# Optimization experiments

Hardware: AMD Instinct MI355X
Metric: run time of the kernel (lower is better)

## Reference

```python
import jax, jax.numpy as jnp
import numpy as np

B, N, DIM, H = 4, 128, 512, 8
EPS = 1e-5

def _lin(k, fan_in, fan_out):
    kw, kb = jax.random.split(k)
    w = jax.random.normal(kw, (fan_in, fan_out), jnp.float32) * 0.02
    b = jax.random.normal(kb, (fan_out,), jnp.float32) * 0.02
    return w, b

def setup_inputs() -> dict:
    key = jax.random.key(0)
    ks = jax.random.split(key, 12)
    node_features = jax.random.normal(ks[0], (B, N, DIM), jnp.float32)
    edge_features = jax.random.normal(ks[1], (B, N, N, DIM), jnp.float32)
    adjacency_weights = jax.random.uniform(ks[2], (B, N, N), jnp.float32)
    Wn_w, Wn_b = _lin(ks[3], DIM, DIM)
    We1_w, We1_b = _lin(ks[4], 3 * DIM, DIM)
    We2_w, We2_b = _lin(ks[5], DIM, H)
    Wm_w, Wm_b = _lin(ks[6], DIM, DIM)
    Wu1_w, Wu1_b = _lin(ks[7], 3 * DIM, DIM)
    Wu2_w, Wu2_b = _lin(ks[8], DIM, DIM)
    Wo_w, Wo_b = _lin(ks[9], DIM, DIM)
    ln_g = jnp.ones((DIM,), jnp.float32)
    ln_b = jnp.zeros((DIM,), jnp.float32)
    return dict(node_features=node_features, edge_features=edge_features,
                adjacency_weights=adjacency_weights,
                Wn_w=Wn_w, Wn_b=Wn_b, We1_w=We1_w, We1_b=We1_b,
                We2_w=We2_w, We2_b=We2_b, Wm_w=Wm_w, Wm_b=Wm_b,
                Wu1_w=Wu1_w, Wu1_b=Wu1_b, Wu2_w=Wu2_w, Wu2_b=Wu2_b,
                Wo_w=Wo_w, Wo_b=Wo_b, ln_g=ln_g, ln_b=ln_b)

def _layernorm(x, g, b):
    mu = jnp.mean(x, axis=-1, keepdims=True)
    var = jnp.var(x, axis=-1, keepdims=True)
    return (x - mu) * jax.lax.rsqrt(var + EPS) * g + b

def reference(node_features, edge_features, adjacency_weights,
              Wn_w, Wn_b, We1_w, We1_b, We2_w, We2_b, Wm_w, Wm_b,
              Wu1_w, Wu1_b, Wu2_w, Wu2_b, Wo_w, Wo_b, ln_g, ln_b):
    b, n, d = node_features.shape
    h = node_features @ Wn_w + Wn_b                       # (B,N,D)
    h_i = jnp.broadcast_to(h[:, :, None, :], (b, n, n, d))
    h_j = jnp.broadcast_to(h[:, None, :, :], (b, n, n, d))
    edge_input = jnp.concatenate([h_i, h_j, edge_features], axis=-1)  # (B,N,N,3D)
    # edge attention MLP
    e = jax.nn.leaky_relu(edge_input @ We1_w + We1_b, negative_slope=0.2)
    attn = e @ We2_w + We2_b                              # (B,N,N,H)
    attn = jax.nn.softmax(attn, axis=2)                   # softmax over j
    attn = attn * adjacency_weights[..., None]
    # messages: W_msg applied to h_j == W_msg(h) broadcast; aggregate with mean attn
    messages = h @ Wm_w + Wm_b                            # (B,N,D)
    attn_mean = jnp.mean(attn, axis=-1)                   # (B,N,N)
    aggregated = jnp.einsum('bij,bjd->bid', attn_mean, messages)
    updated_nodes = _layernorm(node_features + (aggregated @ Wo_w + Wo_b), ln_g, ln_b)
    # edge update MLP (exact GELU as in torch default)
    u = jax.nn.gelu(edge_input @ Wu1_w + Wu1_b, approximate=False)
    updated_edges = edge_features + (u @ Wu2_w + Wu2_b)
    return updated_nodes, updated_edges
```

## Files before the change

### kernel.cpp

```cpp
#include <hip/hip_runtime.h>
#include <hip/hip_bf16.h>


typedef __bf16  bf16x8 __attribute__((ext_vector_type(8)));
typedef float   f32x4  __attribute__((ext_vector_type(4)));
typedef __hip_bfloat16 bfloat;

#define AS1 __attribute__((address_space(1)))
#define AS3 __attribute__((address_space(3)))

__device__ __forceinline__ void g2l16(const void* g, void* l) {
  __builtin_amdgcn_global_load_lds((AS1 void*)g, (AS3 void*)l, 16, 0, 0);
}

__device__ __forceinline__ float ldf(const void* p, size_t i, int f) {
  return f ? ((const float*)p)[i] : __bfloat162float(((const bfloat*)p)[i]);
}
__device__ __forceinline__ void stf(void* p, size_t i, float v, int f) {
  if (f) ((float*)p)[i] = v;
  else   ((bfloat*)p)[i] = __float2bfloat16(v);
}

__device__ __forceinline__ float gelu_f(float x) {
  float y = 0.7978845608028654f * (x + 0.044715f * x * x * x);
  float e = __expf(2.0f * y);
  float t = 1.0f - 2.0f / (e + 1.0f);
  return 0.5f * x * (1.0f + t);
}

__global__ __launch_bounds__(256) void detect_dtype(const unsigned short* nu, int* flag) {
  __shared__ int bad;
  if (threadIdx.x == 0) bad = 0;
  __syncthreads();
  int local = 0;
  for (int i = threadIdx.x; i < 4096; i += 256) {
    int ex = (nu[i] >> 7) & 0xFF;
    if (ex >= 0xC0) local = 1;
  }
  if (local) atomicOr(&bad, 1);
  __syncthreads();
  if (threadIdx.x == 0) *flag = bad;
}

__global__ __launch_bounds__(256) void cvt_edge(const float* E, const int* flag, void* dout) {
  if (*flag == 0) return;
  const int e = blockIdx.x & 7;
  const int x = blockIdx.x >> 3;
  const int m = x >> 5;
  const int h = (x >> 4) & 1;
  const int s = x & 15;
  const int c = 2 * e + 16 * m + h;
  const int t = threadIdx.x;
  const int rloc = s * 4 + (t >> 6);
  const int c8 = t & 63;
  const float* src = E + ((size_t)c * 64 + rloc) * 512 + (size_t)c8 * 8;
  f32x4 lo = *(const f32x4*)src;
  f32x4 hi = *(const f32x4*)(src + 4);
  bf16x8 v;
  v[0] = (__bf16)lo[0]; v[1] = (__bf16)lo[1]; v[2] = (__bf16)lo[2]; v[3] = (__bf16)lo[3];
  v[4] = (__bf16)hi[0]; v[5] = (__bf16)hi[1]; v[6] = (__bf16)hi[2]; v[7] = (__bf16)hi[3];
  char* eb = (char*)dout + 1048576;
  *(bf16x8*)(eb + (size_t)c * 131072 + (size_t)rloc * 1024 + (size_t)c8 * 16) = v;
}

__global__ __launch_bounds__(256) void transpose3(const void* We1, const void* Wu1,
                                                  const void* Wu2, const int* flag,
                                                  bfloat* WtA, bfloat* WtB, bfloat* WtC) {
  const int f = *flag;
  int idx = blockIdx.x * 256 + threadIdx.x;
  int m = idx >> 18;
  int r = idx & 262143;
  int n = r >> 9, k = r & 511;
  size_t si = (size_t)k * 512 + n;
  float v;
  bfloat* dst;
  if (m == 0)      { v = ldf(We1, 524288 + si, f); dst = WtA; }
  else if (m == 1) { v = ldf(Wu1, 524288 + si, f); dst = WtB; }
  else             { v = ldf(Wu2, si, f);          dst = WtC; }
  dst[(size_t)n * 512 + k] = __float2bfloat16(v);
}

__global__ __launch_bounds__(256) void small_gemm(const void* A, int amode, const void* W,
                                                  size_t woff, const void* bias,
                                                  const int* flag, float* out) {
  const int f = *flag;
  const int af = amode ? 1 : f;
  __shared__ float sA[4][512];
  const int t = threadIdx.x;
  const int r0 = blockIdx.x * 4;
  for (int idx = t; idx < 2048; idx += 256)
    sA[idx >> 9][idx & 511] = ldf(A, (size_t)(r0 + (idx >> 9)) * 512 + (idx & 511), af);
  __syncthreads();
  float acc0[4] = {0.f, 0.f, 0.f, 0.f}, acc1[4] = {0.f, 0.f, 0.f, 0.f};
#pragma unroll 4
  for (int k = 0; k < 512; ++k) {
    float w0 = ldf(W, woff + (size_t)k * 512 + t, f);
    float w1 = ldf(W, woff + (size_t)k * 512 + t + 256, f);
#pragma unroll
    for (int r = 0; r < 4; ++r) {
      acc0[r] += sA[r][k] * w0;
      acc1[r] += sA[r][k] * w1;
    }
  }
  float b0 = bias ? ldf(bias, t, f) : 0.f;
  float b1 = bias ? ldf(bias, t + 256, f) : 0.f;
#pragma unroll
  for (int r = 0; r < 4; ++r) {
    out[(size_t)(r0 + r) * 512 + t] = acc0[r] + b0;
    out[(size_t)(r0 + r) * 512 + t + 256] = acc1[r] + b1;
  }
}

__global__ __launch_bounds__(256) void fused5(const float* h, const void* We1, const void* We1b,
                                              const void* Wu1, const void* Wu1b, const void* Wm,
                                              const void* Wmb, const int* flag, float* P1,
                                              float* Q1, float* P2, float* Q2, float* msgv) {
  const int f = *flag;
  const void* W;
  size_t woff = 0;
  const void* bias = nullptr;
  float* out;
  switch (blockIdx.y) {
    case 0:  W = We1; bias = We1b; out = P1; break;
    case 1:  W = We1; woff = 262144; out = Q1; break;
    case 2:  W = Wu1; bias = Wu1b; out = P2; break;
    case 3:  W = Wu1; woff = 262144; out = Q2; break;
    default: W = Wm;  bias = Wmb;  out = msgv; break;
  }
  __shared__ float sA[4][512];
  const int t = threadIdx.x;
  const int r0 = blockIdx.x * 4;
  for (int idx = t; idx < 2048; idx += 256)
    sA[idx >> 9][idx & 511] = h[(size_t)(r0 + (idx >> 9)) * 512 + (idx & 511)];
  __syncthreads();
  float acc0[4] = {0.f, 0.f, 0.f, 0.f}, acc1[4] = {0.f, 0.f, 0.f, 0.f};
#pragma unroll 4
  for (int k = 0; k < 512; ++k) {
    float w0 = ldf(W, woff + (size_t)k * 512 + t, f);
    float w1 = ldf(W, woff + (size_t)k * 512 + t + 256, f);
#pragma unroll
    for (int r = 0; r < 4; ++r) {
      acc0[r] += sA[r][k] * w0;
      acc1[r] += sA[r][k] * w1;
    }
  }
  float b0 = bias ? ldf(bias, t, f) : 0.f;
  float b1 = bias ? ldf(bias, t + 256, f) : 0.f;
#pragma unroll
  for (int r = 0; r < 4; ++r) {
    out[(size_t)(r0 + r) * 512 + t] = acc0[r] + b0;
    out[(size_t)(r0 + r) * 512 + t + 256] = acc1[r] + b1;
  }
}

__global__ __launch_bounds__(256) void k3_edge_mlp(const void* E, const bfloat* WtA,
                                                   const bfloat* WtB, const float* P1,
                                                   const float* Q1, const float* P2,
                                                   const float* Q2, const void* We2,
                                                   const int* flag, float* logits4, void* dout) {
  const int f = *flag;
  __shared__ __align__(16) char smem[53248];
  f32x4 acc[4][4];
#pragma unroll
  for (int mi = 0; mi < 4; ++mi)
#pragma unroll
    for (int ni = 0; ni < 4; ++ni) acc[mi][ni] = (f32x4){0.f, 0.f, 0.f, 0.f};

  const int idx0 = blockIdx.x;
  const int bm = (idx0 >> 6) * 8 + (idx0 & 7);
  const int bn = (idx0 >> 3) & 7;
  const bool attn = bn < 4;
  const bfloat* Bg = attn ? WtA + (size_t)bn * 65536 : WtB + (size_t)(bn - 4) * 65536;
  const bfloat* Eb = (const bfloat*)E;
  const char* eb = (const char*)dout + 1048576;

  const int t = threadIdx.x;
  const int lane = t & 63;
  const int wave = t >> 6;
  const int wrow = wave >> 1, wcol = wave & 1;
  const int l15 = lane & 15;
  const int q = lane >> 4;
  const int blockcol = (attn ? bn : (bn - 4)) * 128;

  const int row0 = t >> 2, p0 = t & 3, g0 = p0 ^ (row0 & 3);
  const int row1 = 64 + row0, g1 = p0 ^ (row1 & 3);
  const char* srcB0 = (const char*)Bg + ((size_t)row0 * 512 + g0 * 8) * 2;
  const char* srcB1 = (const char*)Bg + ((size_t)row1 * 512 + g1 * 8) * 2;
  const char* srcA0;
  const char* srcA1;
  const int gr0 = bm * 128 + row0, gr1 = gr0 + 64;
  if (f) {
    srcA0 = eb + (size_t)(gr0 >> 6) * 131072 + (size_t)(gr0 & 63) * 1024 + (size_t)g0 * 16;
    srcA1 = eb + (size_t)(gr1 >> 6) * 131072 + (size_t)(gr1 & 63) * 1024 + (size_t)g1 * 16;
  } else {
    srcA0 = (const char*)Eb + ((size_t)gr0 * 512 + g0 * 8) * 2;
    srcA1 = (const char*)Eb + ((size_t)gr1 * 512 + g1 * 8) * 2;
  }
  const int dst0 = wave * 1024;
  const int dst1 = 4096 + wave * 1024;

  auto stage = [&](int kt2, int sel2) {
    char* dA = smem + sel2 * 8192;
    char* dB = smem + 24576 + sel2 * 8192;
    const int koff = kt2 * 64;
    g2l16(srcA0 + koff, dA + dst0);
    g2l16(srcA1 + koff, dA + dst1);
    g2l16(srcB0 + koff, dB + dst0);
    g2l16(srcB1 + koff, dB + dst1);
  };

  stage(0, 0);
  stage(1, 1);

  if (attn) {
    for (int idx = t; idx < 2048; idx += 256) {
      const int n = idx >> 7, k = idx & 127;
      float v = (n < 8) ? ldf(We2, (size_t)(blockcol + k) * 8 + n, f) : 0.f;
      *(bfloat*)(smem + 49152 + (size_t)n * 256 + (((k >> 3) ^ n) * 16) + (k & 7) * 2) =
          __float2bfloat16(v);
    }
  }

  const int fA = (wrow * 64 + l15) * 64 + ((q ^ (l15 & 3)) * 16);
  const int fB = (wcol * 64 + l15) * 64 + ((q ^ (l15 & 3)) * 16);

#pragma unroll
  for (int kt = 0; kt < 16; ++kt) {
    if (kt < 15) asm volatile("s_waitcnt vmcnt(4)" ::: "memory");
    else         asm volatile("s_waitcnt vmcnt(0)" ::: "memory");
    __builtin_amdgcn_s_barrier();
    if (kt < 14) stage(kt + 2, (kt + 2) % 3);
    const char* A = smem + (kt % 3) * 8192;
    const char* B = smem + 24576 + (kt % 3) * 8192;
    bf16x8 afr[4], bfr[4];
#pragma unroll
    for (int mi = 0; mi < 4; ++mi) afr[mi] = *(const bf16x8*)(A + fA + mi * 1024);
#pragma unroll
    for (int ni = 0; ni < 4; ++ni) bfr[ni] = *(const bf16x8*)(B + fB + ni * 1024);
#pragma unroll
    for (int mi = 0; mi < 4; ++mi)
#pragma unroll
      for (int ni = 0; ni < 4; ++ni)
        acc[mi][ni] =
            __builtin_amdgcn_mfma_f32_16x16x32_bf16(afr[mi], bfr[ni], acc[mi][ni], 0, 0, 0);
  }

  const int b = bm >> 7;
  const float* P = attn ? P1 : P2;
  const float* Qm = attn ? Q1 : Q2;
  float pv[4];
#pragma unroll
  for (int ni = 0; ni < 4; ++ni)
    pv[ni] = P[(size_t)bm * 512 + blockcol + wcol * 64 + ni * 16 + l15];

  __syncthreads();

  if (!attn) {
#pragma unroll
    for (int mi = 0; mi < 4; ++mi)
#pragma unroll
      for (int rr = 0; rr < 4; ++rr) {
        const int j = wrow * 64 + mi * 16 + q * 4 + rr;
#pragma unroll
        for (int ni = 0; ni < 4; ++ni) {
          const int cc = wcol * 64 + ni * 16 + l15;
          const int c = blockcol + cc;
          float x = acc[mi][ni][rr] + pv[ni] + Qm[((size_t)b * 128 + j) * 512 + c];
          *(bfloat*)(smem + (size_t)j * 256 + (((cc >> 3) ^ (j & 15)) * 16) + (cc & 7) * 2) =
              __float2bfloat16(gelu_f(x));
        }
      }
    __syncthreads();
    char* ubase = (char*)dout + (f ? (1048576 + 65536) : 524288);
    const size_t blkstride = f ? 131072 : 65536;
#pragma unroll
    for (int rd = 0; rd < 8; ++rd) {
      const int j = rd * 16 + (t >> 4);
      const int ch = t & 15;
      f32x4 v = *(const f32x4*)(smem + (size_t)j * 256 + ((ch ^ (j & 15)) * 16));
      const size_t m = (size_t)bm * 128 + j;
      *(f32x4*)(ubase + (m >> 6) * blkstride + (m & 63) * 1024 + (size_t)blockcol * 2 +
                (size_t)ch * 16) = v;
    }
  } else {
#pragma unroll
    for (int mi = 0; mi < 4; ++mi)
#pragma unroll
      for (int rr = 0; rr < 4; ++rr) {
        const int j = wrow * 64 + mi * 16 + q * 4 + rr;
#pragma unroll
        for (int ni = 0; ni < 4; ++ni) {
          const int cc = wcol * 64 + ni * 16 + l15;
          const int c = blockcol + cc;
          float x = acc[mi][ni][rr] + pv[ni] + Qm[((size_t)b * 128 + j) * 512 + c];
          float e4 = (x >= 0.f) ? x : 0.2f * x;
          *(bfloat*)(smem + (size_t)j * 256 + (((cc >> 3) ^ (j & 15)) * 16) + (cc & 7) * 2) =
              __float2bfloat16(e4);
        }
      }
    __syncthreads();
    f32x4 acc2[2];
    acc2[0] = (f32x4){0.f, 0.f, 0.f, 0.f};
    acc2[1] = (f32x4){0.f, 0.f, 0.f, 0.f};
    const int jb = wave * 32;
#pragma unroll
    for (int ks = 0; ks < 4; ++ks) {
      const int gA = ((ks * 4 + q) ^ l15) * 16;
      bf16x8 a0 = *(const bf16x8*)(smem + (size_t)(jb + l15) * 256 + gA);
      bf16x8 a1 = *(const bf16x8*)(smem + (size_t)(jb + 16 + l15) * 256 + gA);
      bf16x8 bb = *(const bf16x8*)(smem + 49152 + (size_t)l15 * 256 + gA);
      acc2[0] = __builtin_amdgcn_mfma_f32_16x16x32_bf16(a0, bb, acc2[0], 0, 0, 0);
      acc2[1] = __builtin_amdgcn_mfma_f32_16x16x32_bf16(a1, bb, acc2[1], 0, 0, 0);
    }
#pragma unroll
    for (int mi2 = 0; mi2 < 2; ++mi2)
#pragma unroll
      for (int rr = 0; rr < 4; ++rr) {
        if (l15 < 8) {
          const int j = jb + mi2 * 16 + q * 4 + rr;
          logits4[(((size_t)bn * 512 + bm) * 128 + j) * 8 + l15] = acc2[mi2][rr];
        }
      }
  }
}

__global__ __launch_bounds__(512) void k6_edge_out(const bfloat* WtC, const void* Wu2b,
                                                   const void* E, const int* flag, void* dout) {
  const int f = *flag;
  __shared__ __align__(16) char smem[36864];
  char* sA = smem;
  char* sB = smem + 4096;
  f32x4 acc[2][8];
#pragma unroll
  for (int mi = 0; mi < 2; ++mi)
#pragma unroll
    for (int ni = 0; ni < 8; ++ni) acc[mi][ni] = (f32x4){0.f, 0.f, 0.f, 0.f};

  const int e = blockIdx.x & 7;
  const int x = blockIdx.x >> 3;
  const int bm = 2 * e + 16 * (x >> 1) + (x & 1);
  const int t = threadIdx.x;
  const int lane = t & 63;
  const int wave = t >> 6;
  const int wm = wave >> 2, wn = wave & 3;
  const int l15 = lane & 15;
  const int q = lane >> 4;
  const size_t r0 = (size_t)bm * 64;
  const char* ua = (const char*)dout +
                   (f ? (1048576 + (size_t)bm * 131072 + 65536) : (524288 + (size_t)bm * 65536));

  for (int kt = 0; kt < 16; ++kt) {
    __syncthreads();
    const int k0 = kt * 32;
    if (t < 256) {
      const int row = t >> 2;
      const int gseg = (t & 3) ^ ((row >> 1) & 3);
      g2l16(ua + (size_t)row * 1024 + (size_t)(k0 + gseg * 8) * 2, sA + wave * 64 * 16);
    }
#pragma unroll
    for (int c = 0; c < 4; ++c) {
      const int idx = c * 512 + t;
      const int row = idx >> 2;
      const int gseg = (idx & 3) ^ ((row >> 1) & 3);
      g2l16(WtC + (size_t)row * 512 + k0 + gseg * 8, sB + (c * 512 + wave * 64) * 16);
    }
    __syncthreads();
    bf16x8 afr[2], bfr[8];
#pragma unroll
    for (int mi = 0; mi < 2; ++mi) {
      const int r = wm * 32 + mi * 16 + l15;
      afr[mi] = *(const bf16x8*)(sA + ((size_t)r * 32 + (q ^ ((r >> 1) & 3)) * 8) * 2);
    }
#pragma unroll
    for (int ni = 0; ni < 8; ++ni) {
      const int r = wn * 128 + ni * 16 + l15;
      bfr[ni] = *(const bf16x8*)(sB + ((size_t)r * 32 + (q ^ ((r >> 1) & 3)) * 8) * 2);
    }
#pragma unroll
    for (int mi = 0; mi < 2; ++mi)
#pragma unroll
      for (int ni = 0; ni < 8; ++ni)
        acc[mi][ni] = __builtin_amdgcn_mfma_f32_16x16x32_bf16(afr[mi], bfr[ni], acc[mi][ni], 0, 0, 0);
  }
  float wb[8];
#pragma unroll
  for (int ni = 0; ni < 8; ++ni) wb[ni] = ldf(Wu2b, wn * 128 + ni * 16 + l15, f);
  const bfloat* eres = (const bfloat*)((const char*)dout + 1048576 + (size_t)bm * 131072);
#pragma unroll
  for (int mi = 0; mi < 2; ++mi)
#pragma unroll
    for (int rr = 0; rr < 4; ++rr) {
      const int j = wm * 32 + mi * 16 + q * 4 + rr;
#pragma unroll
      for (int ni = 0; ni < 8; ++ni) {
        const int c = wn * 128 + ni * 16 + l15;
        float r = f ? __bfloat162float(eres[(size_t)j * 512 + c])
                    : __bfloat162float(((const bfloat*)E)[(r0 + j) * 512 + c]);
        acc[mi][ni][rr] += wb[ni] + r;
      }
    }
  __syncthreads();
#pragma unroll
  for (int mi = 0; mi < 2; ++mi)
#pragma unroll
    for (int rr = 0; rr < 4; ++rr) {
      const int j = wm * 32 + mi * 16 + q * 4 + rr;
      const size_t row = r0 + j;
#pragma unroll
      for (int ni = 0; ni < 8; ++ni) {
        const int c = wn * 128 + ni * 16 + l15;
        stf(dout, 262144 + row * 512 + c, acc[mi][ni][rr], f);
      }
    }
}

__global__ __launch_bounds__(128) void softmax_mean(const float* logits4, const void* adj,
                                                    const int* flag, float* amean) {
  const int f = *flag;
  const int bi = blockIdx.x;
  const int j = threadIdx.x;
  __shared__ float red[128];
  float macc = 0.f;
  for (int hh = 0; hh < 8; ++hh) {
    float x = 0.f;
#pragma unroll
    for (int s = 0; s < 4; ++s)
      x += logits4[(((size_t)s * 512 + bi) * 128 + j) * 8 + hh];
    red[j] = x;
    __syncthreads();
    for (int s = 64; s > 0; s >>= 1) {
      if (j < s) red[j] = fmaxf(red[j], red[j + s]);
      __syncthreads();
    }
    float mx = red[0];
    __syncthreads();
    float ex = __expf(x - mx);
    red[j] = ex;
    __syncthreads();
    for (int s = 64; s > 0; s >>= 1) {
      if (j < s) red[j] += red[j + s];
      __syncthreads();
    }
    float sum = red[0];
    __syncthreads();
    macc += ex / sum;
  }
  amean[(size_t)bi * 128 + j] = macc * 0.125f * ldf(adj, (size_t)bi * 128 + j, f);
}

__global__ __launch_bounds__(256) void node_fused(const float* amean, const float* msg,
                                                  const void* Wo, const void* Wob,
                                                  const void* node, const void* lng,
                                                  const void* lnb, const int* flag, void* dout) {
  const int f = *flag;
  const int bi = blockIdx.x;
  const int b = bi >> 7;
  const int t = threadIdx.x;
  __shared__ float am[128];
  __shared__ float sAgg[512];
  __shared__ float red[256];
  if (t < 128) am[t] = amean[(size_t)bi * 128 + t];
  __syncthreads();
  float a0 = 0.f, a1 = 0.f;
#pragma unroll 4
  for (int jj = 0; jj < 128; ++jj) {
    const float* mr = msg + ((size_t)b * 128 + jj) * 512;
    a0 += am[jj] * mr[t];
    a1 += am[jj] * mr[t + 256];
  }
  sAgg[t] = a0;
  sAgg[t + 256] = a1;
  __syncthreads();
  float v0 = 0.f, v1 = 0.f;
#pragma unroll 4
  for (int k = 0; k < 512; ++k) {
    float a = sAgg[k];
    v0 += a * ldf(Wo, (size_t)k * 512 + t, f);
    v1 += a * ldf(Wo, (size_t)k * 512 + t + 256, f);
  }
  v0 += ldf(Wob, t, f) + ldf(node, (size_t)bi * 512 + t, f);
  v1 += ldf(Wob, t + 256, f) + ldf(node, (size_t)bi * 512 + t + 256, f);
  red[t] = v0 + v1;
  __syncthreads();
  for (int s = 128; s > 0; s >>= 1) {
    if (t < s) red[t] += red[t + s];
    __syncthreads();
  }
  float mean = red[0] * (1.f / 512.f);
  __syncthreads();
  red[t] = (v0 - mean) * (v0 - mean) + (v1 - mean) * (v1 - mean);
  __syncthreads();
  for (int s = 128; s > 0; s >>= 1) {
    if (t < s) red[t] += red[t + s];
    __syncthreads();
  }
  float var = red[0] * (1.f / 512.f);
  float inv = rsqrtf(var + 1e-5f);
  stf(dout, (size_t)bi * 512 + t, (v0 - mean) * inv * ldf(lng, t, f) + ldf(lnb, t, f), f);
  stf(dout, (size_t)bi * 512 + t + 256,
      (v1 - mean) * inv * ldf(lng, t + 256, f) + ldf(lnb, t + 256, f), f);
}

extern "C" void kernel_launch(void* const* d_in, const int* in_sizes, int n_in, void* d_out,
                              int out_size, void* d_ws, size_t ws_size, hipStream_t stream) {
  (void)in_sizes; (void)n_in; (void)out_size; (void)ws_size;
  const void* node = d_in[0];
  const void* edge = d_in[1];
  const void* adj = d_in[2];
  const void* Wn_w = d_in[3];
  const void* Wn_b = d_in[4];
  const void* We1_w = d_in[5];
  const void* We1_b = d_in[6];
  const void* We2_w = d_in[7];
  const void* Wm_w = d_in[9];
  const void* Wm_b = d_in[10];
  const void* Wu1_w = d_in[11];
  const void* Wu1_b = d_in[12];
  const void* Wu2_w = d_in[13];
  const void* Wu2_b = d_in[14];
  const void* Wo_w = d_in[15];
  const void* Wo_b = d_in[16];
  const void* ln_g = d_in[17];
  const void* ln_b = d_in[18];

  char* w = (char*)d_ws;
  int* flag = (int*)w;        w += 256;
  float* h = (float*)w;       w += 262144 * 4;
  float* P1 = (float*)w;      w += 262144 * 4;
  float* Q1 = (float*)w;      w += 262144 * 4;
  float* P2 = (float*)w;      w += 262144 * 4;
  float* Q2 = (float*)w;      w += 262144 * 4;
  float* msg = (float*)w;     w += 262144 * 4;
  float* logits4 = (float*)w; w += (size_t)4 * 524288 * 4;
  float* amean = (float*)w;   w += 65536 * 4;
  bfloat* WtA = (bfloat*)w;   w += 262144 * 2;
  bfloat* WtB = (bfloat*)w;   w += 262144 * 2;
  bfloat* WtC = (bfloat*)w;   w += 262144 * 2;

  detect_dtype<<<1, 256, 0, stream>>>((const unsigned short*)node, flag);
  cvt_edge<<<16384, 256, 0, stream>>>((const float*)edge, flag, d_out);
  transpose3<<<3072, 256, 0, stream>>>(We1_w, Wu1_w, Wu2_w, flag, WtA, WtB, WtC);
  small_gemm<<<128, 256, 0, stream>>>(node, 0, Wn_w, 0, Wn_b, flag, h);
  fused5<<<dim3(128, 5), 256, 0, stream>>>(h, We1_w, We1_b, Wu1_w, Wu1_b, Wm_w, Wm_b, flag,
                                           P1, Q1, P2, Q2, msg);
  k3_edge_mlp<<<4096, 256, 0, stream>>>(edge, WtA, WtB, P1, Q1, P2, Q2, We2_w, flag,
                                        logits4, d_out);
  softmax_mean<<<512, 128, 0, stream>>>(logits4, adj, flag, amean);
  node_fused<<<512, 256, 0, stream>>>(amean, msg, Wo_w, Wo_b, node, ln_g, ln_b, flag, d_out);
  k6_edge_out<<<1024, 512, 0, stream>>>(WtC, Wu2_b, edge, flag, d_out);
}
```

Measured before the change: 752.8 us.

## Triple-buffer edge-out GEMM loads, tweak LDS swizzle, warp-shuffle softmax reduction

The edge-output GEMM kernel moves from a two-barrier synchronous load loop to a 3-stage global-to-LDS pipeline with vmcnt waits and precomputed fragment offsets, so loads overlap the MFMA work. Its LDS use grows to about 108 KB, which may limit occupancy. The edge GEMM's swizzle now XORs with (row>>1)&3 instead of row&3, to cut LDS bank conflicts. The softmax-mean kernel replaces eight sequential shared-memory tree reductions with vectorized logit loads and wave shuffle reductions across all 8 heads at once.

```diff
diff --git a/kernel.cpp b/kernel.cpp
--- a/kernel.cpp
+++ b/kernel.cpp
@@ -182,8 +182,8 @@
   const int q = lane >> 4;
   const int blockcol = (attn ? bn : (bn - 4)) * 128;
 
-  const int row0 = t >> 2, p0 = t & 3, g0 = p0 ^ (row0 & 3);
-  const int row1 = 64 + row0, g1 = p0 ^ (row1 & 3);
+  const int row0 = t >> 2, p0 = t & 3, g0 = p0 ^ ((row0 >> 1) & 3);
+  const int row1 = 64 + row0, g1 = p0 ^ ((row1 >> 1) & 3);
   const char* srcB0 = (const char*)Bg + ((size_t)row0 * 512 + g0 * 8) * 2;
   const char* srcB1 = (const char*)Bg + ((size_t)row1 * 512 + g1 * 8) * 2;
   const char* srcA0;
@@ -221,8 +221,8 @@
     }
   }
 
-  const int fA = (wrow * 64 + l15) * 64 + ((q ^ (l15 & 3)) * 16);
-  const int fB = (wcol * 64 + l15) * 64 + ((q ^ (l15 & 3)) * 16);
+  const int fA = (wrow * 64 + l15) * 64 + ((q ^ ((l15 >> 1) & 3)) * 16);
+  const int fB = (wcol * 64 + l15) * 64 + ((q ^ ((l15 >> 1) & 3)) * 16);
 
 #pragma unroll
   for (int kt = 0; kt < 16; ++kt) {
@@ -327,9 +327,7 @@
 __global__ __launch_bounds__(512) void k6_edge_out(const bfloat* WtC, const void* Wu2b,
                                                    const void* E, const int* flag, void* dout) {
   const int f = *flag;
-  __shared__ __align__(16) char smem[36864];
-  char* sA = smem;
-  char* sB = smem + 4096;
+  __shared__ __align__(16) char smem[110592];
   f32x4 acc[2][8];
 #pragma unroll
   for (int mi = 0; mi < 2; ++mi)
@@ -349,33 +347,49 @@
   const char* ua = (const char*)dout +
                    (f ? (1048576 + (size_t)bm * 131072 + 65536) : (524288 + (size_t)bm * 65536));
 
+  const int iA = t & 255;
+  const int rowA = iA >> 2, pA = iA & 3, gA = pA ^ ((rowA >> 1) & 3);
+  const char* srcA = ua + (size_t)rowA * 1024 + (size_t)gA * 16;
+  const int dstA = (wave & 3) * 1024;
+  const char* srcB[4];
+  int dstB[4];
+#pragma unroll
+  for (int c = 0; c < 4; ++c) {
+    const int idx = c * 512 + t;
+    const int row = idx >> 2, p = idx & 3, g = p ^ ((row >> 1) & 3);
+    srcB[c] = (const char*)WtC + ((size_t)row * 512 + g * 8) * 2;
+    dstB[c] = (c * 512 + wave * 64) * 16;
+  }
+
+  auto stage = [&](int kt2, int sel2) {
+    const int koff = kt2 * 64;
+    char* dA = smem + sel2 * 4096;
+    char* dB = smem + 12288 + sel2 * 32768;
+    g2l16(srcA + koff, dA + dstA);
+#pragma unroll
+    for (int c = 0; c < 4; ++c) g2l16(srcB[c] + koff, dB + dstB[c]);
+  };
+
+  stage(0, 0);
+  stage(1, 1);
+
+  const int swz = (q ^ ((l15 >> 1) & 3)) * 16;
+  const int fAo = (wm * 32 + l15) * 64 + swz;
+  const int fBo = (wn * 128 + l15) * 64 + swz;
+
+#pragma unroll
   for (int kt = 0; kt < 16; ++kt) {
-    __syncthreads();
-    const int k0 = kt * 32;
-    if (t < 256) {
-      const int row = t >> 2;
-      const int gseg = (t & 3) ^ ((row >> 1) & 3);
-      g2l16(ua + (size_t)row * 1024 + (size_t)(k0 + gseg * 8) * 2, sA + wave * 64 * 16);
-    }
-#pragma unroll
-    for (int c = 0; c < 4; ++c) {
-      const int idx = c * 512 + t;
-      const int row = idx >> 2;
-      const int gseg = (idx & 3) ^ ((row >> 1) & 3);
-      g2l16(WtC + (size_t)row * 512 + k0 + gseg * 8, sB + (c * 512 + wave * 64) * 16);
-    }
-    __syncthreads();
+    if (kt < 15) asm volatile("s_waitcnt vmcnt(5)" ::: "memory");
+    else         asm volatile("s_waitcnt vmcnt(0)" ::: "memory");
+    __builtin_amdgcn_s_barrier();
+    if (kt < 14) stage(kt + 2, (kt + 2) % 3);
+    const char* sA = smem + (kt % 3) * 4096;
+    const char* sB = smem + 12288 + (kt % 3) * 32768;
     bf16x8 afr[2], bfr[8];
 #pragma unroll
-    for (int mi = 0; mi < 2; ++mi) {
-      const int r = wm * 32 + mi * 16 + l15;
-      afr[mi] = *(const bf16x8*)(sA + ((size_t)r * 32 + (q ^ ((r >> 1) & 3)) * 8) * 2);
-    }
-#pragma unroll
-    for (int ni = 0; ni < 8; ++ni) {
-      const int r = wn * 128 + ni * 16 + l15;
-      bfr[ni] = *(const bf16x8*)(sB + ((size_t)r * 32 + (q ^ ((r >> 1) & 3)) * 8) * 2);
-    }
+    for (int mi = 0; mi < 2; ++mi) afr[mi] = *(const bf16x8*)(sA + fAo + mi * 1024);
+#pragma unroll
+    for (int ni = 0; ni < 8; ++ni) bfr[ni] = *(const bf16x8*)(sB + fBo + ni * 1024);
 #pragma unroll
     for (int mi = 0; mi < 2; ++mi)
 #pragma unroll
@@ -419,32 +433,49 @@
   const int f = *flag;
   const int bi = blockIdx.x;
   const int j = threadIdx.x;
-  __shared__ float red[128];
+  const int wv = j >> 6;
+  __shared__ float sred[2][8];
+  f32x4 v0 = (f32x4){0.f, 0.f, 0.f, 0.f}, v1 = (f32x4){0.f, 0.f, 0.f, 0.f};
+#pragma unroll
+  for (int s = 0; s < 4; ++s) {
+    const float* p = logits4 + (((size_t)s * 512 + bi) * 128 + j) * 8;
+    v0 += *(const f32x4*)p;
+    v1 += *(const f32x4*)(p + 4);
+  }
+  float xv[8], m[8];
+#pragma unroll
+  for (int k = 0; k < 4; ++k) { xv[k] = v0[k]; xv[4 + k] = v1[k]; }
+#pragma unroll
+  for (int h = 0; h < 8; ++h) m[h] = xv[h];
+#pragma unroll
+  for (int o = 1; o < 64; o <<= 1)
+#pragma unroll
+    for (int h = 0; h < 8; ++h) m[h] = fmaxf(m[h], __shfl_xor(m[h], o));
+  if ((j & 63) == 0) {
+#pragma unroll
+    for (int h = 0; h < 8; ++h) sred[wv][h] = m[h];
+  }
+  __syncthreads();
+  float ex[8], s8[8];
+#pragma unroll
+  for (int h = 0; h < 8; ++h) {
+    float mx = fmaxf(sred[0][h], sred[1][h]);
+    ex[h] = __expf(xv[h] - mx);
+    s8[h] = ex[h];
+  }
+#pragma unroll
+  for (int o = 1; o < 64; o <<= 1)
+#pragma unroll
+    for (int h = 0; h < 8; ++h) s8[h] += __shfl_xor(s8[h], o);
+  __syncthreads();
+  if ((j & 63) == 0) {
+#pragma unroll
+    for (int h = 0; h < 8; ++h) sred[wv][h] = s8[h];
+  }
+  __syncthreads();
   float macc = 0.f;
-  for (int hh = 0; hh < 8; ++hh) {
-    float x = 0.f;
-#pragma unroll
-    for (int s = 0; s < 4; ++s)
-      x += logits4[(((size_t)s * 512 + bi) * 128 + j) * 8 + hh];
-    red[j] = x;
-    __syncthreads();
-    for (int s = 64; s > 0; s >>= 1) {
-      if (j < s) red[j] = fmaxf(red[j], red[j + s]);
-      __syncthreads();
-    }
-    float mx = red[0];
-    __syncthreads();
-    float ex = __expf(x - mx);
-    red[j] = ex;
-    __syncthreads();
-    for (int s = 64; s > 0; s >>= 1) {
-      if (j < s) red[j] += red[j + s];
-      __syncthreads();
-    }
-    float sum = red[0];
-    __syncthreads();
-    macc += ex / sum;
-  }
+#pragma unroll
+  for (int h = 0; h < 8; ++h) macc += ex[h] / (sred[0][h] + sred[1][h]);
   amean[(size_t)bi * 128 + j] = macc * 0.125f * ldf(adj, (size_t)bi * 128 + j, f);
 }
 
```

Measured after the change: 732.8 us. 1.03x faster.
